# Kernel optimization log

Measured on AMD Instinct MI355X. Metric: run time of the kernel, lower is better.

## Reference

```python
import jax, jax.numpy as jnp
import numpy as np

N, E, C, H = 50000, 800000, 64, 64  # nodes, edges, channels, mlp hidden


def _seg_softmax(logits, seg, num_segments):
    # per-destination-node, per-channel softmax over incoming edges (PyG softmax)
    m = jax.ops.segment_max(logits, seg, num_segments=num_segments)
    m = jnp.where(jnp.isfinite(m), m, 0.0)
    e = jnp.exp(logits - m[seg])
    s = jax.ops.segment_sum(e, seg, num_segments=num_segments)
    return e / (s[seg] + 1e-16)


def setup_inputs() -> dict:
    key = jax.random.key(0)
    ks = jax.random.split(key, 16)

    def w(k, shape, fan_in):
        lim = 1.0 / np.sqrt(fan_in)
        return jax.random.uniform(k, shape, jnp.float32, -lim, lim)

    return dict(
        x=jax.random.normal(ks[0], (N, C), jnp.float32),
        pos=jax.random.uniform(ks[1], (N, 3), jnp.float32),
        edge_index=jax.random.randint(ks[2], (2, E), 0, N),
        # lin_in (Linear with bias)
        W_in=w(ks[3], (C, C), C), b_in=jnp.zeros((C,), jnp.float32),
        # PointTransformerConv internal linears (bias=False in PyG)
        W_lin=w(ks[4], (C, C), C),
        W_src=w(ks[5], (C, C), C),
        W_dst=w(ks[6], (C, C), C),
        # pos_nn: Linear(3,64) + ReLU + Linear(64,C)
        Wp1=w(ks[7], (3, H), 3), bp1=jnp.zeros((H,), jnp.float32),
        Wp2=w(ks[8], (H, C), H), bp2=jnp.zeros((C,), jnp.float32),
        # attn_nn: Linear(C,64) + ReLU + Linear(64,C)
        Wa1=w(ks[9], (C, H), C), ba1=jnp.zeros((H,), jnp.float32),
        Wa2=w(ks[10], (H, C), H), ba2=jnp.zeros((C,), jnp.float32),
        # lin_out
        W_out=w(ks[11], (C, C), C), b_out=jnp.zeros((C,), jnp.float32),
    )


def reference(x, pos, edge_index, W_in, b_in, W_lin, W_src, W_dst,
              Wp1, bp1, Wp2, bp2, Wa1, ba1, Wa2, ba2, W_out, b_out):
    n = x.shape[0]
    src, dst = edge_index[0], edge_index[1]
    # lin_in + ReLU
    h = jax.nn.relu(x @ W_in + b_in)                      # [N,C]
    # PointTransformerConv projections
    v = h @ W_lin                                         # values [N,C]
    a_src = h @ W_src                                     # alpha_j source term
    a_dst = h @ W_dst                                     # alpha_i dest term
    # per-edge positional encoding: pos_nn(pos_i - pos_j)
    rel = pos[dst] - pos[src]                             # [E,3]
    delta = jax.nn.relu(rel @ Wp1 + bp1) @ Wp2 + bp2      # [E,C]
    # attention logits: attn_nn(alpha_i - alpha_j + delta)
    alpha = a_dst[dst] - a_src[src] + delta               # [E,C]
    alpha = jax.nn.relu(alpha @ Wa1 + ba1) @ Wa2 + ba2    # [E,C]
    alpha = _seg_softmax(alpha, dst, n)
    # weighted scatter-sum aggregation: sum_j alpha * (x_j + delta)
    out = jax.ops.segment_sum(alpha * (v[src] + delta), dst, num_segments=n)
    # lin_out + ReLU
    return jax.nn.relu(out @ W_out + b_out)
```

## Files before the change

### kernel.cpp

```cpp
#include <hip/hip_runtime.h>

typedef unsigned short u16;
typedef unsigned int   u32;
typedef unsigned long long u64;
typedef __attribute__((ext_vector_type(8))) short bf16x8;
typedef __attribute__((ext_vector_type(4))) float f32x4;

#define DEV static __device__ __forceinline__

DEV u16 f2bf(float f){ union{float f; u32 i;} v; v.f=f; u32 u=v.i;
                       return (u16)((u + 0x7FFFu + ((u>>16)&1u))>>16); }
DEV float bf2f(u16 u){ union{u32 i; float f;} v; v.i=((u32)u)<<16; return v.f; }
DEV float bfl(u32 w){ return bf2f((u16)(w & 0xffffu)); }
DEV float bfh(u32 w){ return bf2f((u16)(w >> 16)); }
DEV u32 pk2(float a, float b){ return (u32)f2bf(a) | ((u32)f2bf(b) << 16); }
DEV void ldsfence(){ asm volatile("s_waitcnt lgkmcnt(0)" ::: "memory"); }

#define NBIAS 384
#define FB_P1 0
#define FB_P2 4
#define FB_A1 12
#define FB_A2 20
#define FB_IN 28
#define FB_LIN 36
#define FB_SRC 44
#define FB_DST 52
#define FB_OUT 60
#define NFRAG 68

#define LROW 70
#define LROWD 35

DEV bf16x8 fb_load(const u16* __restrict__ FB, int frag, int lane){
  union{ uint4 u; bf16x8 v; } w;
  w.u = *(const uint4*)(FB + ((size_t)(frag*64+lane))*8);
  return w.v;
}
DEV bf16x8 lds_read_chunk(const u32* l32, int dw){
  union{ u32 d[4]; bf16x8 v; } u;
#pragma unroll
  for(int p=0;p<4;p++) u.d[p] = l32[dw+p];
  return u.v;
}

__global__ __launch_bounds__(256) void k_fuse(
  const float* __restrict__ Wsrc, const float* __restrict__ Wdst,
  const float* __restrict__ Wp2,  const float* __restrict__ Wa1,
  const float* __restrict__ bp2,  const float* __restrict__ ba1,
  float* __restrict__ Wsa, float* __restrict__ Wda,
  float* __restrict__ Wp2a1, float* __restrict__ batt1)
{
  int b = blockIdx.x, tid = threadIdx.x;
  if(b < 3){
    const float* A = (b==0)? Wsrc : (b==1)? Wdst : Wp2;
    float* O       = (b==0)? Wsa  : (b==1)? Wda  : Wp2a1;
    for(int o = tid; o < 4096; o += 256){
      int i = o >> 6, j = o & 63;
      float s = 0.f;
      for(int k=0;k<64;k++) s += A[i*64+k] * Wa1[k*64+j];
      O[o] = s;
    }
  } else {
    if(tid < 64){
      float s = ba1[tid];
      for(int k=0;k<64;k++) s += bp2[k] * Wa1[k*64+tid];
      batt1[tid] = s;
    }
  }
}

__global__ __launch_bounds__(256) void k_prep(
  const float* __restrict__ Win, const float* __restrict__ Wlin,
  const float* __restrict__ Wsrc, const float* __restrict__ Wdst,
  const float* __restrict__ Wp1, const float* __restrict__ Wp2,
  const float* __restrict__ Wa1, const float* __restrict__ Wa2,
  const float* __restrict__ Wout,
  const float* __restrict__ bin, const float* __restrict__ bp1, const float* __restrict__ bp2,
  const float* __restrict__ ba1, const float* __restrict__ ba2, const float* __restrict__ bout,
  float* __restrict__ Bf, u16* __restrict__ FB)
{
  int idx = blockIdx.x*256 + threadIdx.x;
  if(idx < NBIAS){
    int which = idx >> 6, c = idx & 63;
    const float* b;
    switch(which){ case 0:b=bin;break; case 1:b=bp1;break; case 2:b=bp2;break;
                   case 3:b=ba1;break; case 4:b=ba2;break; default:b=bout;break; }
    Bf[idx] = b[c];
  } else if(idx < NBIAS + NFRAG*64){
    int j = idx - NBIAS;
    int frag = j >> 6, lane = j & 63;
    int t = lane & 15, q = lane >> 4;
    const float* src; int K = 64, nt, s;
    if(frag < 4){ src = Wp1; K = 3; nt = frag; s = 0; }
    else if(frag < 12){ int g=frag-4;  src=Wp2;  nt=g>>1; s=g&1; }
    else if(frag < 20){ int g=frag-12; src=Wa1;  nt=g>>1; s=g&1; }
    else if(frag < 28){ int g=frag-20; src=Wa2;  nt=g>>1; s=g&1; }
    else if(frag < 36){ int g=frag-28; src=Win;  nt=g>>1; s=g&1; }
    else if(frag < 44){ int g=frag-36; src=Wlin; nt=g>>1; s=g&1; }
    else if(frag < 52){ int g=frag-44; src=Wsrc; nt=g>>1; s=g&1; }
    else if(frag < 60){ int g=frag-52; src=Wdst; nt=g>>1; s=g&1; }
    else              { int g=frag-60; src=Wout; nt=g>>1; s=g&1; }
    u16* dst = FB + ((size_t)(frag*64+lane))*8;
#pragma unroll
    for(int jj=0;jj<8;jj++){
      int k = s*32 + q*8 + jj;
      dst[jj] = (k<K) ? f2bf(src[k*64 + nt*16 + t]) : (u16)0;
    }
  }
}

__global__ __launch_bounds__(256) void k_node_m(
  const float* __restrict__ x, const float* __restrict__ Bf, const u16* __restrict__ FB,
  u16* __restrict__ vf, u16* __restrict__ asof, u16* __restrict__ adof,
  int N, int ntiles)
{
  __shared__ u16 sc16[4][16*LROW];
  int lane = threadIdx.x & 63, warp = threadIdx.x >> 6;
  int t = lane & 15, q = lane >> 4;
  int tile = blockIdx.x*4 + warp;
  if(tile >= ntiles) return;
  u16* lb = sc16[warp]; u32* lb32 = (u32*)lb;
  int r0 = tile*16;
  int row = r0 + t; if(row >= N) row = N-1;

  const float4* x4 = (const float4*)(x + (size_t)row*64);
  bf16x8 xa[2];
#pragma unroll
  for(int s=0;s<2;s++){
    float4 u0 = x4[s*8 + q*2], u1 = x4[s*8 + q*2 + 1];
    xa[s][0]=(short)f2bf(u0.x); xa[s][1]=(short)f2bf(u0.y);
    xa[s][2]=(short)f2bf(u0.z); xa[s][3]=(short)f2bf(u0.w);
    xa[s][4]=(short)f2bf(u1.x); xa[s][5]=(short)f2bf(u1.y);
    xa[s][6]=(short)f2bf(u1.z); xa[s][7]=(short)f2bf(u1.w);
  }
  f32x4 zero = {0.f,0.f,0.f,0.f};
  f32x4 acc[4];
#pragma unroll
  for(int nt=0;nt<4;nt++){
    acc[nt] = __builtin_amdgcn_mfma_f32_16x16x32_bf16(xa[0], fb_load(FB, FB_IN+nt*2+0, lane), zero, 0,0,0);
    acc[nt] = __builtin_amdgcn_mfma_f32_16x16x32_bf16(xa[1], fb_load(FB, FB_IN+nt*2+1, lane), acc[nt], 0,0,0);
  }
#pragma unroll
  for(int nt=0;nt<4;nt++)
#pragma unroll
    for(int r=0;r<4;r++)
      lb[(q*4+r)*LROW + nt*16 + t] = f2bf(fmaxf(acc[nt][r] + Bf[nt*16+t], 0.f));
  ldsfence();
  bf16x8 h0 = lds_read_chunk(lb32, t*LROWD + q*4);
  bf16x8 h1 = lds_read_chunk(lb32, t*LROWD + 16 + q*4);

  const int fb0[3] = {FB_LIN, FB_SRC, FB_DST};
  u16* Os[3] = {vf, asof, adof};
#pragma unroll
  for(int mtx=0; mtx<3; mtx++){
    f32x4 av[4];
#pragma unroll
    for(int nt=0;nt<4;nt++){
      av[nt] = __builtin_amdgcn_mfma_f32_16x16x32_bf16(h0, fb_load(FB, fb0[mtx]+nt*2+0, lane), zero, 0,0,0);
      av[nt] = __builtin_amdgcn_mfma_f32_16x16x32_bf16(h1, fb_load(FB, fb0[mtx]+nt*2+1, lane), av[nt], 0,0,0);
    }
    u16* O = Os[mtx];
#pragma unroll
    for(int r=0;r<4;r++){
      int rr = r0 + q*4 + r;
      if(rr < N){
        uint2 o;
        o.x = (u32)f2bf(av[0][r]) | ((u32)f2bf(av[1][r]) << 16);
        o.y = (u32)f2bf(av[2][r]) | ((u32)f2bf(av[3][r]) << 16);
        *(uint2*)(O + (size_t)rr*64 + t*4) = o;
      }
    }
  }
}

__global__ __launch_bounds__(256) void k_hist(const int* __restrict__ ei, int* __restrict__ deg, int E){
  int e = blockIdx.x*256 + threadIdx.x;
  if(e < E) atomicAdd(&deg[ei[(size_t)E + e]], 1);
}

__global__ __launch_bounds__(256) void k_scanA(const int* __restrict__ deg,
    int* __restrict__ row_start, int* __restrict__ bsum, int N){
  __shared__ int b[256];
  int tid = threadIdx.x, i = blockIdx.x*256 + tid;
  int v = (i<N) ? deg[i] : 0;
  b[tid] = v; __syncthreads();
#pragma unroll
  for(int off=1; off<256; off<<=1){
    int u = (tid>=off) ? b[tid-off] : 0;
    __syncthreads(); b[tid] += u; __syncthreads();
  }
  if(i<N) row_start[i] = b[tid] - v;
  if(tid==255) bsum[blockIdx.x] = b[255];
}
__global__ __launch_bounds__(256) void k_scanB(int* __restrict__ bsum,
    int* __restrict__ bsoff, int* __restrict__ row_start, int nb, int N){
  __shared__ int b[256];
  int tid = threadIdx.x;
  int v = (tid<nb) ? bsum[tid] : 0;
  b[tid] = v; __syncthreads();
#pragma unroll
  for(int off=1; off<256; off<<=1){
    int u = (tid>=off) ? b[tid-off] : 0;
    __syncthreads(); b[tid] += u; __syncthreads();
  }
  if(tid<nb) bsoff[tid] = b[tid] - v;
  if(tid==255) row_start[N] = b[255];
}
__global__ __launch_bounds__(256) void k_scanC(int* __restrict__ row_start,
    const int* __restrict__ bsoff, int N){
  int i = blockIdx.x*256 + threadIdx.x;
  if(i<N) row_start[i] += bsoff[blockIdx.x];
}

__global__ __launch_bounds__(256) void k_scatter(const int* __restrict__ ei,
    const int* __restrict__ row_start, int* __restrict__ cursor,
    int2* __restrict__ pair, int E){
  int e = blockIdx.x*256 + threadIdx.x;
  if(e >= E) return;
  int d = ei[(size_t)E + e];
  int p = atomicAdd(&cursor[d], 1);
  int2 pr; pr.x = ei[e]; pr.y = d;
  pair[row_start[d] + p] = pr;
}

DEV void flushseg(int d, float* numP, float* SP, const int* __restrict__ row_start,
                  float* __restrict__ num, float* __restrict__ S,
                  int lo, int hi, int q, int t){
  if(d < 0) return;
#pragma unroll
  for(int nt=0;nt<4;nt++){
    numP[nt] += __shfl_xor(numP[nt], 16, 64);
    numP[nt] += __shfl_xor(numP[nt], 32, 64);
    SP[nt]   += __shfl_xor(SP[nt],   16, 64);
    SP[nt]   += __shfl_xor(SP[nt],   32, 64);
  }
  bool partial = (row_start[d] < lo) || (row_start[d+1] > hi);
  if(q==0){
#pragma unroll
    for(int nt=0;nt<4;nt++){
      size_t off = (size_t)d*64 + nt*16 + t;
      if(partial){ atomicAdd(&num[off], numP[nt]); atomicAdd(&S[off], SP[nt]); }
      else       { num[off] = numP[nt]; S[off] = SP[nt]; }
    }
  }
#pragma unroll
  for(int nt=0;nt<4;nt++){ numP[nt]=0.f; SP[nt]=0.f; }
}

DEV void agg_tile(int tbase, int hi_w, int lo_w, int did,
                  const float wv[4][4], const float pd[4][4],
                  int& cur_d, float* numP, float* SP,
                  const int* __restrict__ row_start,
                  float* __restrict__ num, float* __restrict__ S, int q, int t){
  int m = 0;
  while(m < 16){
    int d0 = __shfl(did, m, 64);
    u32 same = (u32)(__ballot(did == d0) & 0xFFFFull);
    u32 rest = ~(same >> m);
    int len = __ffs(rest) - 1;
    int m1 = m + len;
    if(d0 != cur_d){
      flushseg(cur_d, numP, SP, row_start, num, S, lo_w, hi_w, q, t);
      cur_d = d0;
    }
#pragma unroll
    for(int r=0;r<4;r++){
      int mm = q*4 + r;
      bool use = (mm >= m) && (mm < m1) && ((tbase+mm) < hi_w);
      if(use){
#pragma unroll
        for(int nt=0;nt<4;nt++){
          numP[nt] += wv[nt][r] * pd[r][nt];
          SP[nt]   += wv[nt][r];
        }
      }
    }
    m = m1;
  }
}

__global__ __launch_bounds__(256,2) void k_edge_p3(
  const int* __restrict__ row_start, const int2* __restrict__ pair,
  const float* __restrict__ pos, const float* __restrict__ Bf, const u16* __restrict__ FB,
  const u16* __restrict__ vf, const u16* __restrict__ asof, const u16* __restrict__ adof,
  float* __restrict__ S, float* __restrict__ num, int E, int nsuper, int spw)
{
  __shared__ u16 sc16[4][32*LROW];
  int lane = threadIdx.x & 63, warp = threadIdx.x >> 6;
  int t = lane & 15, q = lane >> 4;
  int wid = blockIdx.x*4 + warp;
  int s0 = wid*spw, s1 = s0 + spw;
  if(s0 >= nsuper) return;
  if(s1 > nsuper) s1 = nsuper;
  int lo = s0*32, hi = s1*32; if(hi > E) hi = E;
  u16* lb = sc16[warp]; u32* lb32 = (u32*)lb;

  float bp1f[4], bp2f[4], baf[4], ba2f[4];
#pragma unroll
  for(int nt=0;nt<4;nt++){
    bp1f[nt]=Bf[ 64+nt*16+t]; bp2f[nt]=Bf[128+nt*16+t];
    baf[nt] =Bf[192+nt*16+t]; ba2f[nt]=Bf[256+nt*16+t];
  }
  const uint2* ad2 = (const uint2*)adof;
  const uint2* as2 = (const uint2*)asof;
  const uint2* v2  = (const uint2*)vf;
  f32x4 zero = {0.f,0.f,0.f,0.f};
  float numP[4] = {0,0,0,0}, SP[4] = {0,0,0,0};
  int cur_d = -1;

  for(int tb = lo; tb < hi; tb += 32){
    bool hasB = (tb+16) < hi;
    int ecA = tb + t;        if(ecA >= hi) ecA = hi-1;
    int ecB = tb + 16 + t;   if(ecB >= hi) ecB = hi-1;
    int2 spA = pair[ecA], spB = pair[ecB];
    int sidA = spA.x, didA = spA.y;
    int sidB = spB.x, didB = spB.y;

    bf16x8 a1A, a1B;
#pragma unroll
    for(int j=0;j<8;j++){ a1A[j]=0; a1B[j]=0; }
    if(q==0){
      a1A[0] = (short)f2bf(pos[(size_t)didA*3+0] - pos[(size_t)sidA*3+0]);
      a1A[1] = (short)f2bf(pos[(size_t)didA*3+1] - pos[(size_t)sidA*3+1]);
      a1A[2] = (short)f2bf(pos[(size_t)didA*3+2] - pos[(size_t)sidA*3+2]);
      a1B[0] = (short)f2bf(pos[(size_t)didB*3+0] - pos[(size_t)sidB*3+0]);
      a1B[1] = (short)f2bf(pos[(size_t)didB*3+1] - pos[(size_t)sidB*3+1]);
      a1B[2] = (short)f2bf(pos[(size_t)didB*3+2] - pos[(size_t)sidB*3+2]);
    }
    f32x4 accA[4], accB[4];
#pragma unroll
    for(int nt=0;nt<4;nt++){
      bf16x8 wp = fb_load(FB, FB_P1+nt, lane);
      accA[nt] = __builtin_amdgcn_mfma_f32_16x16x32_bf16(a1A, wp, zero, 0,0,0);
      accB[nt] = __builtin_amdgcn_mfma_f32_16x16x32_bf16(a1B, wp, zero, 0,0,0);
    }

    ldsfence();
#pragma unroll
    for(int nt=0;nt<4;nt++)
#pragma unroll
      for(int r=0;r<4;r++){
        lb[(     q*4+r)*LROW + nt*16 + t] = f2bf(fmaxf(accA[nt][r] + bp1f[nt], 0.f));
        lb[(16 + q*4+r)*LROW + nt*16 + t] = f2bf(fmaxf(accB[nt][r] + bp1f[nt], 0.f));
      }
    ldsfence();

    uint2 adwA[4], aswA[4], adwB[4], aswB[4];
#pragma unroll
    for(int r=0;r<4;r++){
      int mm = q*4 + r;
      int dA = __shfl(didA, mm, 64), sA = __shfl(sidA, mm, 64);
      int dB = __shfl(didB, mm, 64), sB = __shfl(sidB, mm, 64);
      adwA[r] = ad2[(size_t)dA*16 + t];
      aswA[r] = as2[(size_t)sA*16 + t];
      adwB[r] = ad2[(size_t)dB*16 + t];
      aswB[r] = as2[(size_t)sB*16 + t];
    }

    bf16x8 atA0 = lds_read_chunk(lb32, (t   )*LROWD + q*4);
    bf16x8 atA1 = lds_read_chunk(lb32, (t   )*LROWD + 16 + q*4);
    bf16x8 atB0 = lds_read_chunk(lb32, (t+16)*LROWD + q*4);
    bf16x8 atB1 = lds_read_chunk(lb32, (t+16)*LROWD + 16 + q*4);

    u32 dpA[4][2], dpB[4][2];
#pragma unroll
    for(int nt=0;nt<4;nt++){
      bf16x8 w0 = fb_load(FB, FB_P2+nt*2+0, lane);
      bf16x8 w1 = fb_load(FB, FB_P2+nt*2+1, lane);
      f32x4 a = __builtin_amdgcn_mfma_f32_16x16x32_bf16(atA0, w0, zero, 0,0,0);
      a = __builtin_amdgcn_mfma_f32_16x16x32_bf16(atA1, w1, a, 0,0,0);
      f32x4 b = __builtin_amdgcn_mfma_f32_16x16x32_bf16(atB0, w0, zero, 0,0,0);
      b = __builtin_amdgcn_mfma_f32_16x16x32_bf16(atB1, w1, b, 0,0,0);
      dpA[nt][0] = pk2(a[0]+bp2f[nt], a[1]+bp2f[nt]);
      dpA[nt][1] = pk2(a[2]+bp2f[nt], a[3]+bp2f[nt]);
      dpB[nt][0] = pk2(b[0]+bp2f[nt], b[1]+bp2f[nt]);
      dpB[nt][1] = pk2(b[2]+bp2f[nt], b[3]+bp2f[nt]);
    }

    ldsfence();
#pragma unroll
    for(int nt=0;nt<4;nt++){
      bf16x8 w0 = fb_load(FB, FB_A1+nt*2+0, lane);
      bf16x8 w1 = fb_load(FB, FB_A1+nt*2+1, lane);
      f32x4 a = __builtin_amdgcn_mfma_f32_16x16x32_bf16(atA0, w0, zero, 0,0,0);
      a = __builtin_amdgcn_mfma_f32_16x16x32_bf16(atA1, w1, a, 0,0,0);
#pragma unroll
      for(int r=0;r<4;r++){
        u32 dw = (nt&2)? adwA[r].y : adwA[r].x;
        u32 sw = (nt&2)? aswA[r].y : aswA[r].x;
        float c = ((nt&1)? bfh(dw) : bfl(dw)) - ((nt&1)? bfh(sw) : bfl(sw));
        lb[(q*4+r)*LROW + nt*16 + t] = f2bf(fmaxf(a[r] + c + baf[nt], 0.f));
      }
    }
#pragma unroll
    for(int nt=0;nt<4;nt++){
      bf16x8 w0 = fb_load(FB, FB_A1+nt*2+0, lane);
      bf16x8 w1 = fb_load(FB, FB_A1+nt*2+1, lane);
      f32x4 b = __builtin_amdgcn_mfma_f32_16x16x32_bf16(atB0, w0, zero, 0,0,0);
      b = __builtin_amdgcn_mfma_f32_16x16x32_bf16(atB1, w1, b, 0,0,0);
#pragma unroll
      for(int r=0;r<4;r++){
        u32 dw = (nt&2)? adwB[r].y : adwB[r].x;
        u32 sw = (nt&2)? aswB[r].y : aswB[r].x;
        float c = ((nt&1)? bfh(dw) : bfl(dw)) - ((nt&1)? bfh(sw) : bfl(sw));
        lb[(16 + q*4+r)*LROW + nt*16 + t] = f2bf(fmaxf(b[r] + c + baf[nt], 0.f));
      }
    }
    ldsfence();

    uint2 vrawA[4], vrawB[4];
#pragma unroll
    for(int r=0;r<4;r++){
      int mm = q*4 + r;
      int sA = __shfl(sidA, mm, 64);
      int sB = __shfl(sidB, mm, 64);
      vrawA[r] = v2[(size_t)sA*16 + t];
      vrawB[r] = v2[(size_t)sB*16 + t];
    }

    bf16x8 auA0 = lds_read_chunk(lb32, (t   )*LROWD + q*4);
    bf16x8 auA1 = lds_read_chunk(lb32, (t   )*LROWD + 16 + q*4);
    bf16x8 auB0 = lds_read_chunk(lb32, (t+16)*LROWD + q*4);
    bf16x8 auB1 = lds_read_chunk(lb32, (t+16)*LROWD + 16 + q*4);

    float wv[4][4], pd[4][4];
#pragma unroll
    for(int nt=0;nt<4;nt++){
      bf16x8 w0 = fb_load(FB, FB_A2+nt*2+0, lane);
      bf16x8 w1 = fb_load(FB, FB_A2+nt*2+1, lane);
      f32x4 a = __builtin_amdgcn_mfma_f32_16x16x32_bf16(auA0, w0, zero, 0,0,0);
      a = __builtin_amdgcn_mfma_f32_16x16x32_bf16(auA1, w1, a, 0,0,0);
#pragma unroll
      for(int r=0;r<4;r++)
        wv[nt][r] = ((tb + q*4 + r) < hi) ? __expf(fminf(a[r] + ba2f[nt], 80.f)) : 0.f;
    }
#pragma unroll
    for(int r=0;r<4;r++){
      float va[4] = { bfl(vrawA[r].x), bfh(vrawA[r].x), bfl(vrawA[r].y), bfh(vrawA[r].y) };
#pragma unroll
      for(int nt=0;nt<4;nt++){
        u32 dw = dpA[nt][r>>1];
        pd[r][nt] = va[nt] + ((r&1)? bfh(dw) : bfl(dw));
      }
    }
    agg_tile(tb, hi, lo, didA, wv, pd, cur_d, numP, SP, row_start, num, S, q, t);

    if(hasB){
#pragma unroll
      for(int nt=0;nt<4;nt++){
        bf16x8 w0 = fb_load(FB, FB_A2+nt*2+0, lane);
        bf16x8 w1 = fb_load(FB, FB_A2+nt*2+1, lane);
        f32x4 b = __builtin_amdgcn_mfma_f32_16x16x32_bf16(auB0, w0, zero, 0,0,0);
        b = __builtin_amdgcn_mfma_f32_16x16x32_bf16(auB1, w1, b, 0,0,0);
#pragma unroll
        for(int r=0;r<4;r++)
          wv[nt][r] = ((tb + 16 + q*4 + r) < hi) ? __expf(fminf(b[r] + ba2f[nt], 80.f)) : 0.f;
      }
#pragma unroll
      for(int r=0;r<4;r++){
        float vb[4] = { bfl(vrawB[r].x), bfh(vrawB[r].x), bfl(vrawB[r].y), bfh(vrawB[r].y) };
#pragma unroll
        for(int nt=0;nt<4;nt++){
          u32 dw = dpB[nt][r>>1];
          pd[r][nt] = vb[nt] + ((r&1)? bfh(dw) : bfl(dw));
        }
      }
      agg_tile(tb+16, hi, lo, didB, wv, pd, cur_d, numP, SP, row_start, num, S, q, t);
    }
  }
  flushseg(cur_d, numP, SP, row_start, num, S, lo, hi, q, t);
}

__global__ __launch_bounds__(256) void k_out_m(
  const float* __restrict__ num, const float* __restrict__ S,
  const float* __restrict__ Bf, const u16* __restrict__ FB,
  float* __restrict__ out, int N, int ntiles)
{
  int lane = threadIdx.x & 63, warp = threadIdx.x >> 6;
  int t = lane & 15, q = lane >> 4;
  int tile = blockIdx.x*4 + warp;
  if(tile >= ntiles) return;
  int r0 = tile*16;
  int row = r0 + t; if(row >= N) row = N-1;
  const float4* n4 = (const float4*)(num + (size_t)row*64);
  const float4* s4 = (const float4*)(S   + (size_t)row*64);
  bf16x8 af[2];
#pragma unroll
  for(int s=0;s<2;s++){
    float4 n0 = n4[s*8 + q*2], n1 = n4[s*8 + q*2 + 1];
    float4 s0 = s4[s*8 + q*2], s1 = s4[s*8 + q*2 + 1];
    af[s][0]=(short)f2bf(n0.x/(s0.x+1e-16f)); af[s][1]=(short)f2bf(n0.y/(s0.y+1e-16f));
    af[s][2]=(short)f2bf(n0.z/(s0.z+1e-16f)); af[s][3]=(short)f2bf(n0.w/(s0.w+1e-16f));
    af[s][4]=(short)f2bf(n1.x/(s1.x+1e-16f)); af[s][5]=(short)f2bf(n1.y/(s1.y+1e-16f));
    af[s][6]=(short)f2bf(n1.z/(s1.z+1e-16f)); af[s][7]=(short)f2bf(n1.w/(s1.w+1e-16f));
  }
  f32x4 zero = {0.f,0.f,0.f,0.f};
#pragma unroll
  for(int nt=0;nt<4;nt++){
    f32x4 a = __builtin_amdgcn_mfma_f32_16x16x32_bf16(af[0], fb_load(FB, FB_OUT+nt*2+0, lane), zero, 0,0,0);
    a = __builtin_amdgcn_mfma_f32_16x16x32_bf16(af[1], fb_load(FB, FB_OUT+nt*2+1, lane), a, 0,0,0);
    float b = Bf[320 + nt*16 + t];
#pragma unroll
    for(int r=0;r<4;r++){
      int rr = r0 + q*4 + r;
      if(rr < N) out[(size_t)rr*64 + nt*16 + t] = fmaxf(a[r] + b, 0.f);
    }
  }
}

extern "C" void kernel_launch(void* const* d_in, const int* in_sizes, int n_in,
                              void* d_out, int out_size, void* d_ws, size_t ws_size,
                              hipStream_t stream){
  const float* x   =(const float*)d_in[0];
  const float* pos =(const float*)d_in[1];
  const int*   ei  =(const int*)d_in[2];
  const float* Win =(const float*)d_in[3];  const float* bin=(const float*)d_in[4];
  const float* Wlin=(const float*)d_in[5];  const float* Wsrc=(const float*)d_in[6];
  const float* Wdst=(const float*)d_in[7];
  const float* Wp1 =(const float*)d_in[8];  const float* bp1=(const float*)d_in[9];
  const float* Wp2 =(const float*)d_in[10]; const float* bp2=(const float*)d_in[11];
  const float* Wa1 =(const float*)d_in[12]; const float* ba1=(const float*)d_in[13];
  const float* Wa2 =(const float*)d_in[14]; const float* ba2=(const float*)d_in[15];
  const float* Wout=(const float*)d_in[16]; const float* bout=(const float*)d_in[17];
  int N = in_sizes[0]/64;
  int E = in_sizes[2]/2;

  float* Bf    = (float*)d_ws;
  u16*   FB    = (u16*)(Bf + NBIAS);
  float* Wsa   = (float*)(FB + (size_t)NFRAG*64*8);
  float* Wda   = Wsa + 4096;
  float* Wp2a1 = Wda + 4096;
  float* batt1 = Wp2a1 + 4096;
  u16*   vfb   = (u16*)(batt1 + 64);
  u16*   asb   = vfb + (size_t)N*64;
  u16*   adb   = asb + (size_t)N*64;
  float* S     = (float*)(adb + (size_t)N*64);
  float* num   = S    + (size_t)N*64;
  int* deg       = (int*)(num + (size_t)N*64);
  int* cursor    = deg + N;
  int* row_start = cursor + N;
  int* bsum      = row_start + (N+1);
  int* bsoff     = bsum + 256;
  int2* pair     = (int2*)(bsoff + 256);

  int ntiles = (N+15)/16;
  int nsuper = (E+31)/32;
  int total_waves = 4096;
  int spw = (nsuper + total_waves - 1) / total_waves;
  int nwaves = (nsuper + spw - 1) / spw;
  int eblocks = (nwaves + 3) / 4;
  int nscb = (N+255)/256;

  hipMemsetAsync(deg, 0, (size_t)2*N*sizeof(int), stream);
  hipMemsetAsync(S, 0, (size_t)N*64*2*sizeof(float), stream);
  k_fuse<<<dim3(4), dim3(256), 0, stream>>>(Wsrc, Wdst, Wp2, Wa1, bp2, ba1,
                                            Wsa, Wda, Wp2a1, batt1);
  k_prep<<<dim3(19), dim3(256), 0, stream>>>(Win,Wlin,Wsa,Wda,Wp1,Wp2,Wp2a1,Wa2,Wout,
                                             bin,bp1,bp2,batt1,ba2,bout, Bf, FB);
  k_node_m<<<dim3((ntiles+3)/4), dim3(256), 0, stream>>>(x, Bf, FB, vfb, asb, adb, N, ntiles);
  k_hist<<<dim3((E+255)/256), dim3(256), 0, stream>>>(ei, deg, E);
  k_scanA<<<dim3(nscb), dim3(256), 0, stream>>>(deg, row_start, bsum, N);
  k_scanB<<<dim3(1),    dim3(256), 0, stream>>>(bsum, bsoff, row_start, nscb, N);
  k_scanC<<<dim3(nscb), dim3(256), 0, stream>>>(row_start, bsoff, N);
  k_scatter<<<dim3((E+255)/256), dim3(256), 0, stream>>>(ei, row_start, cursor, pair, E);
  k_edge_p3<<<dim3(eblocks), dim3(256), 0, stream>>>(row_start, pair, pos, Bf, FB,
                                                     vfb, asb, adb, S, num, E, nsuper, spw);
  k_out_m<<<dim3((ntiles+3)/4), dim3(256), 0, stream>>>(num, S, Bf, FB, (float*)d_out, N, ntiles);
}
```

Measured before the change: 384.0 us.

## Merge weight-fusion into prep, double-buffer edge LDS, prefetch gathers earlier

Removes the separate k_fuse launch by computing the Wsrc/Wdst/Wp2 x Wa1 products and the fused bias directly inside k_prep. In the edge kernel, each lane loads its own edge pairs instead of using shuffles, issues the gathers for a_dst, a_src and v earlier, and writes to a second LDS buffer so several fences can be dropped. The edge kernel also launches half as many waves, each covering more edges. The trade-offs are more per-lane pair loads, doubled LDS use per block (which may cut occupancy) and less parallelism in the edge kernel.

```diff
diff --git a/kernel.cpp b/kernel.cpp
--- a/kernel.cpp
+++ b/kernel.cpp
@@ -41,32 +41,6 @@
 #pragma unroll
   for(int p=0;p<4;p++) u.d[p] = l32[dw+p];
   return u.v;
-}
-
-__global__ __launch_bounds__(256) void k_fuse(
-  const float* __restrict__ Wsrc, const float* __restrict__ Wdst,
-  const float* __restrict__ Wp2,  const float* __restrict__ Wa1,
-  const float* __restrict__ bp2,  const float* __restrict__ ba1,
-  float* __restrict__ Wsa, float* __restrict__ Wda,
-  float* __restrict__ Wp2a1, float* __restrict__ batt1)
-{
-  int b = blockIdx.x, tid = threadIdx.x;
-  if(b < 3){
-    const float* A = (b==0)? Wsrc : (b==1)? Wdst : Wp2;
-    float* O       = (b==0)? Wsa  : (b==1)? Wda  : Wp2a1;
-    for(int o = tid; o < 4096; o += 256){
-      int i = o >> 6, j = o & 63;
-      float s = 0.f;
-      for(int k=0;k<64;k++) s += A[i*64+k] * Wa1[k*64+j];
-      O[o] = s;
-    }
-  } else {
-    if(tid < 64){
-      float s = ba1[tid];
-      for(int k=0;k<64;k++) s += bp2[k] * Wa1[k*64+tid];
-      batt1[tid] = s;
-    }
-  }
 }
 
 __global__ __launch_bounds__(256) void k_prep(
@@ -82,29 +56,48 @@
   int idx = blockIdx.x*256 + threadIdx.x;
   if(idx < NBIAS){
     int which = idx >> 6, c = idx & 63;
-    const float* b;
-    switch(which){ case 0:b=bin;break; case 1:b=bp1;break; case 2:b=bp2;break;
-                   case 3:b=ba1;break; case 4:b=ba2;break; default:b=bout;break; }
-    Bf[idx] = b[c];
+    if(which == 3){
+      float sacc = ba1[c];
+      for(int k=0;k<64;k++) sacc += bp2[k]*Wa1[k*64+c];
+      Bf[idx] = sacc;
+    } else {
+      const float* b;
+      switch(which){ case 0:b=bin;break; case 1:b=bp1;break; case 2:b=bp2;break;
+                     case 4:b=ba2;break; default:b=bout;break; }
+      Bf[idx] = b[c];
+    }
   } else if(idx < NBIAS + NFRAG*64){
     int j = idx - NBIAS;
     int frag = j >> 6, lane = j & 63;
     int t = lane & 15, q = lane >> 4;
-    const float* src; int K = 64, nt, s;
+    const float* src = nullptr; const float* fuse = nullptr;
+    int K = 64, nt, s;
     if(frag < 4){ src = Wp1; K = 3; nt = frag; s = 0; }
     else if(frag < 12){ int g=frag-4;  src=Wp2;  nt=g>>1; s=g&1; }
-    else if(frag < 20){ int g=frag-12; src=Wa1;  nt=g>>1; s=g&1; }
+    else if(frag < 20){ int g=frag-12; fuse=Wp2; nt=g>>1; s=g&1; }
     else if(frag < 28){ int g=frag-20; src=Wa2;  nt=g>>1; s=g&1; }
     else if(frag < 36){ int g=frag-28; src=Win;  nt=g>>1; s=g&1; }
     else if(frag < 44){ int g=frag-36; src=Wlin; nt=g>>1; s=g&1; }
-    else if(frag < 52){ int g=frag-44; src=Wsrc; nt=g>>1; s=g&1; }
-    else if(frag < 60){ int g=frag-52; src=Wdst; nt=g>>1; s=g&1; }
+    else if(frag < 52){ int g=frag-44; fuse=Wsrc; nt=g>>1; s=g&1; }
+    else if(frag < 60){ int g=frag-52; fuse=Wdst; nt=g>>1; s=g&1; }
     else              { int g=frag-60; src=Wout; nt=g>>1; s=g&1; }
     u16* dst = FB + ((size_t)(frag*64+lane))*8;
-#pragma unroll
-    for(int jj=0;jj<8;jj++){
-      int k = s*32 + q*8 + jj;
-      dst[jj] = (k<K) ? f2bf(src[k*64 + nt*16 + t]) : (u16)0;
+    if(fuse){
+      int col = nt*16 + t;
+#pragma unroll
+      for(int jj=0;jj<8;jj++){
+        int k = s*32 + q*8 + jj;
+        const float* ar = fuse + k*64;
+        float accv = 0.f;
+        for(int m=0;m<64;m++) accv += ar[m] * Wa1[m*64+col];
+        dst[jj] = f2bf(accv);
+      }
+    } else {
+#pragma unroll
+      for(int jj=0;jj<8;jj++){
+        int k = s*32 + q*8 + jj;
+        dst[jj] = (k<K) ? f2bf(src[k*64 + nt*16 + t]) : (u16)0;
+      }
     }
   }
 }
@@ -279,13 +272,13 @@
   }
 }
 
-__global__ __launch_bounds__(256,2) void k_edge_p3(
+__global__ __launch_bounds__(256,2) void k_edge_p4(
   const int* __restrict__ row_start, const int2* __restrict__ pair,
   const float* __restrict__ pos, const float* __restrict__ Bf, const u16* __restrict__ FB,
   const u16* __restrict__ vf, const u16* __restrict__ asof, const u16* __restrict__ adof,
   float* __restrict__ S, float* __restrict__ num, int E, int nsuper, int spw)
 {
-  __shared__ u16 sc16[4][32*LROW];
+  __shared__ u16 sc16[4][2*32*LROW];
   int lane = threadIdx.x & 63, warp = threadIdx.x >> 6;
   int t = lane & 15, q = lane >> 4;
   int wid = blockIdx.x*4 + warp;
@@ -293,7 +286,8 @@
   if(s0 >= nsuper) return;
   if(s1 > nsuper) s1 = nsuper;
   int lo = s0*32, hi = s1*32; if(hi > E) hi = E;
-  u16* lb = sc16[warp]; u32* lb32 = (u32*)lb;
+  u16* lb = sc16[warp];             u32* lb32 = (u32*)lb;
+  u16* lu = sc16[warp] + 32*LROW;   u32* lu32 = (u32*)lu;
 
   float bp1f[4], bp2f[4], baf[4], ba2f[4];
 #pragma unroll
@@ -315,6 +309,13 @@
     int2 spA = pair[ecA], spB = pair[ecB];
     int sidA = spA.x, didA = spA.y;
     int sidB = spB.x, didB = spB.y;
+    int2 prA[4], prB[4];
+#pragma unroll
+    for(int r=0;r<4;r++){
+      int eA = tb + q*4 + r;      if(eA >= hi) eA = hi-1;
+      int eB = tb + 16 + q*4 + r; if(eB >= hi) eB = hi-1;
+      prA[r] = pair[eA]; prB[r] = pair[eB];
+    }
 
     bf16x8 a1A, a1B;
 #pragma unroll
@@ -335,7 +336,6 @@
       accB[nt] = __builtin_amdgcn_mfma_f32_16x16x32_bf16(a1B, wp, zero, 0,0,0);
     }
 
-    ldsfence();
 #pragma unroll
     for(int nt=0;nt<4;nt++)
 #pragma unroll
@@ -344,23 +344,20 @@
         lb[(16 + q*4+r)*LROW + nt*16 + t] = f2bf(fmaxf(accB[nt][r] + bp1f[nt], 0.f));
       }
     ldsfence();
-
-    uint2 adwA[4], aswA[4], adwB[4], aswB[4];
-#pragma unroll
-    for(int r=0;r<4;r++){
-      int mm = q*4 + r;
-      int dA = __shfl(didA, mm, 64), sA = __shfl(sidA, mm, 64);
-      int dB = __shfl(didB, mm, 64), sB = __shfl(sidB, mm, 64);
-      adwA[r] = ad2[(size_t)dA*16 + t];
-      aswA[r] = as2[(size_t)sA*16 + t];
-      adwB[r] = ad2[(size_t)dB*16 + t];
-      aswB[r] = as2[(size_t)sB*16 + t];
-    }
 
     bf16x8 atA0 = lds_read_chunk(lb32, (t   )*LROWD + q*4);
     bf16x8 atA1 = lds_read_chunk(lb32, (t   )*LROWD + 16 + q*4);
     bf16x8 atB0 = lds_read_chunk(lb32, (t+16)*LROWD + q*4);
     bf16x8 atB1 = lds_read_chunk(lb32, (t+16)*LROWD + 16 + q*4);
+
+    uint2 adwA[4], aswA[4], adwB[4], aswB[4];
+#pragma unroll
+    for(int r=0;r<4;r++){
+      adwA[r] = ad2[(size_t)prA[r].y*16 + t];
+      aswA[r] = as2[(size_t)prA[r].x*16 + t];
+      adwB[r] = ad2[(size_t)prB[r].y*16 + t];
+      aswB[r] = as2[(size_t)prB[r].x*16 + t];
+    }
 
     u32 dpA[4][2], dpB[4][2];
 #pragma unroll
@@ -377,7 +374,6 @@
       dpB[nt][1] = pk2(b[2]+bp2f[nt], b[3]+bp2f[nt]);
     }
 
-    ldsfence();
 #pragma unroll
     for(int nt=0;nt<4;nt++){
       bf16x8 w0 = fb_load(FB, FB_A1+nt*2+0, lane);
@@ -389,7 +385,7 @@
         u32 dw = (nt&2)? adwA[r].y : adwA[r].x;
         u32 sw = (nt&2)? aswA[r].y : aswA[r].x;
         float c = ((nt&1)? bfh(dw) : bfl(dw)) - ((nt&1)? bfh(sw) : bfl(sw));
-        lb[(q*4+r)*LROW + nt*16 + t] = f2bf(fmaxf(a[r] + c + baf[nt], 0.f));
+        lu[(q*4+r)*LROW + nt*16 + t] = f2bf(fmaxf(a[r] + c + baf[nt], 0.f));
       }
     }
 #pragma unroll
@@ -403,25 +399,22 @@
         u32 dw = (nt&2)? adwB[r].y : adwB[r].x;
         u32 sw = (nt&2)? aswB[r].y : aswB[r].x;
         float c = ((nt&1)? bfh(dw) : bfl(dw)) - ((nt&1)? bfh(sw) : bfl(sw));
-        lb[(16 + q*4+r)*LROW + nt*16 + t] = f2bf(fmaxf(b[r] + c + baf[nt], 0.f));
-      }
+        lu[(16 + q*4+r)*LROW + nt*16 + t] = f2bf(fmaxf(b[r] + c + baf[nt], 0.f));
+      }
+    }
+
+    uint2 vrawA[4], vrawB[4];
+#pragma unroll
+    for(int r=0;r<4;r++){
+      vrawA[r] = v2[(size_t)prA[r].x*16 + t];
+      vrawB[r] = v2[(size_t)prB[r].x*16 + t];
     }
     ldsfence();
 
-    uint2 vrawA[4], vrawB[4];
-#pragma unroll
-    for(int r=0;r<4;r++){
-      int mm = q*4 + r;
-      int sA = __shfl(sidA, mm, 64);
-      int sB = __shfl(sidB, mm, 64);
-      vrawA[r] = v2[(size_t)sA*16 + t];
-      vrawB[r] = v2[(size_t)sB*16 + t];
-    }
-
-    bf16x8 auA0 = lds_read_chunk(lb32, (t   )*LROWD + q*4);
-    bf16x8 auA1 = lds_read_chunk(lb32, (t   )*LROWD + 16 + q*4);
-    bf16x8 auB0 = lds_read_chunk(lb32, (t+16)*LROWD + q*4);
-    bf16x8 auB1 = lds_read_chunk(lb32, (t+16)*LROWD + 16 + q*4);
+    bf16x8 auA0 = lds_read_chunk(lu32, (t   )*LROWD + q*4);
+    bf16x8 auA1 = lds_read_chunk(lu32, (t   )*LROWD + 16 + q*4);
+    bf16x8 auB0 = lds_read_chunk(lu32, (t+16)*LROWD + q*4);
+    bf16x8 auB1 = lds_read_chunk(lu32, (t+16)*LROWD + 16 + q*4);
 
     float wv[4][4], pd[4][4];
 #pragma unroll
@@ -527,11 +520,7 @@
 
   float* Bf    = (float*)d_ws;
   u16*   FB    = (u16*)(Bf + NBIAS);
-  float* Wsa   = (float*)(FB + (size_t)NFRAG*64*8);
-  float* Wda   = Wsa + 4096;
-  float* Wp2a1 = Wda + 4096;
-  float* batt1 = Wp2a1 + 4096;
-  u16*   vfb   = (u16*)(batt1 + 64);
+  u16*   vfb   = FB + (size_t)NFRAG*64*8;
   u16*   asb   = vfb + (size_t)N*64;
   u16*   adb   = asb + (size_t)N*64;
   float* S     = (float*)(adb + (size_t)N*64);
@@ -545,7 +534,7 @@
 
   int ntiles = (N+15)/16;
   int nsuper = (E+31)/32;
-  int total_waves = 4096;
+  int total_waves = 2048;
   int spw = (nsuper + total_waves - 1) / total_waves;
   int nwaves = (nsuper + spw - 1) / spw;
   int eblocks = (nwaves + 3) / 4;
@@ -553,17 +542,15 @@
 
   hipMemsetAsync(deg, 0, (size_t)2*N*sizeof(int), stream);
   hipMemsetAsync(S, 0, (size_t)N*64*2*sizeof(float), stream);
-  k_fuse<<<dim3(4), dim3(256), 0, stream>>>(Wsrc, Wdst, Wp2, Wa1, bp2, ba1,
-                                            Wsa, Wda, Wp2a1, batt1);
-  k_prep<<<dim3(19), dim3(256), 0, stream>>>(Win,Wlin,Wsa,Wda,Wp1,Wp2,Wp2a1,Wa2,Wout,
-                                             bin,bp1,bp2,batt1,ba2,bout, Bf, FB);
+  k_prep<<<dim3(19), dim3(256), 0, stream>>>(Win,Wlin,Wsrc,Wdst,Wp1,Wp2,Wa1,Wa2,Wout,
+                                             bin,bp1,bp2,ba1,ba2,bout, Bf, FB);
   k_node_m<<<dim3((ntiles+3)/4), dim3(256), 0, stream>>>(x, Bf, FB, vfb, asb, adb, N, ntiles);
   k_hist<<<dim3((E+255)/256), dim3(256), 0, stream>>>(ei, deg, E);
   k_scanA<<<dim3(nscb), dim3(256), 0, stream>>>(deg, row_start, bsum, N);
   k_scanB<<<dim3(1),    dim3(256), 0, stream>>>(bsum, bsoff, row_start, nscb, N);
   k_scanC<<<dim3(nscb), dim3(256), 0, stream>>>(row_start, bsoff, N);
   k_scatter<<<dim3((E+255)/256), dim3(256), 0, stream>>>(ei, row_start, cursor, pair, E);
-  k_edge_p3<<<dim3(eblocks), dim3(256), 0, stream>>>(row_start, pair, pos, Bf, FB,
+  k_edge_p4<<<dim3(eblocks), dim3(256), 0, stream>>>(row_start, pair, pos, Bf, FB,
                                                      vfb, asb, adb, S, num, E, nsuper, spw);
   k_out_m<<<dim3((ntiles+3)/4), dim3(256), 0, stream>>>(num, S, Bf, FB, (float*)d_out, N, ntiles);
 }
```

Result: faster. 359.0 us (-6.5%).
